# Kernel optimization log

Hardware: AMD Instinct MI355X
Metric: run time of the kernel (lower is better)

## Reference

```python
import jax, jax.numpy as jnp
import numpy as np

N_TRACK = 50000
N_LANE = 50000
N_ATT = N_TRACK + N_LANE
NP_T = 1000000
NP_L = 500000
E_ATT = 1600000
D_TRACK = 4
D_LANE = 2
D_ATT = 10
HEADS = 30
D_OUT = 2
EPS = 1e-5
NEG_SLOPE = 0.2


def _mlp(x, W, b, g, beta):
    # Linear -> LayerNorm -> ReLU (matches MLP module)
    h = x @ W + b
    mu = h.mean(-1, keepdims=True)
    var = ((h - mu) ** 2).mean(-1, keepdims=True)
    h = (h - mu) * jax.lax.rsqrt(var + EPS) * g + beta
    return jax.nn.relu(h)


def _seg_max0(x, ids, n):
    # DGL max-reduce; nodes with no in-edges get 0
    m = jax.ops.segment_max(x, ids, num_segments=n, indices_are_sorted=True)
    return jnp.where(jnp.isfinite(m), m, 0.0)


def setup_inputs() -> dict:
    key = jax.random.key(0)
    ks = jax.random.split(key, 16)
    g = lambda i, shape, s=1.0: jax.random.normal(ks[i], shape, jnp.float32) * s
    return {
        'track_point_feats': g(0, (NP_T, D_TRACK)),
        'lane_point_feats': g(1, (NP_L, D_LANE)),
        'point_track_id': jnp.sort(jax.random.randint(ks[2], (NP_T,), 0, N_TRACK)),
        'point_lane_id': jnp.sort(jax.random.randint(ks[3], (NP_L,), 0, N_LANE)),
        'att_src': jax.random.randint(ks[4], (E_ATT,), 0, N_ATT),
        'att_dst': jnp.sort(jax.random.randint(ks[5], (E_ATT,), 0, N_ATT)),
        'track_mlp_W': g(6, (D_TRACK, D_TRACK), 0.5),
        'track_mlp_b': jnp.zeros((D_TRACK,), jnp.float32),
        'track_ln_g': jnp.ones((D_TRACK,), jnp.float32),
        'track_ln_b': jnp.zeros((D_TRACK,), jnp.float32),
        'track_out_W': g(7, (D_TRACK, D_ATT), 0.5),
        'track_out_b': jnp.zeros((D_ATT,), jnp.float32),
        'lane_mlp_W': g(8, (D_LANE, D_LANE), 0.5),
        'lane_mlp_b': jnp.zeros((D_LANE,), jnp.float32),
        'lane_ln_g': jnp.ones((D_LANE,), jnp.float32),
        'lane_ln_b': jnp.zeros((D_LANE,), jnp.float32),
        'lane_out_W': g(9, (D_LANE, D_ATT), 0.5),
        'lane_out_b': jnp.zeros((D_ATT,), jnp.float32),
        'gat_fc_W': g(10, (D_ATT, HEADS * D_OUT), 0.3),
        'gat_attn_l': g(11, (HEADS, D_OUT), 0.3),
        'gat_attn_r': g(12, (HEADS, D_OUT), 0.3),
        'gat_bias': jnp.zeros((HEADS * D_OUT,), jnp.float32),
    }


def reference(track_point_feats, lane_point_feats, point_track_id, point_lane_id,
              att_src, att_dst,
              track_mlp_W, track_mlp_b, track_ln_g, track_ln_b, track_out_W, track_out_b,
              lane_mlp_W, lane_mlp_b, lane_ln_g, lane_ln_b, lane_out_W, lane_out_b,
              gat_fc_W, gat_attn_l, gat_attn_r, gat_bias):
    # SubTrackModel: per-point MLP -> segment max over point->track -> linear
    track_pool = _seg_max0(_mlp(track_point_feats, track_mlp_W, track_mlp_b, track_ln_g, track_ln_b),
                           point_track_id, N_TRACK)
    track_feats = track_pool @ track_out_W + track_out_b  # [N_TRACK, 10]
    # SubLaneModel
    lane_pool = _seg_max0(_mlp(lane_point_feats, lane_mlp_W, lane_mlp_b, lane_ln_g, lane_ln_b),
                          point_lane_id, N_LANE)
    lane_feats = lane_pool @ lane_out_W + lane_out_b  # [N_LANE, 10]
    feats = jnp.concatenate([track_feats, lane_feats], axis=0)  # [N_ATT, 10]

    # GATConv (30 heads, out 2)
    h = (feats @ gat_fc_W).reshape(N_ATT, HEADS, D_OUT)
    el = jnp.einsum('nhd,hd->nh', h, gat_attn_l)
    er = jnp.einsum('nhd,hd->nh', h, gat_attn_r)
    e = jax.nn.leaky_relu(el[att_src] + er[att_dst], NEG_SLOPE)  # [E, H]
    m = jax.ops.segment_max(e, att_dst, num_segments=N_ATT, indices_are_sorted=True)
    m = jnp.where(jnp.isfinite(m), m, 0.0)
    ee = jnp.exp(e - m[att_dst])
    den = jax.ops.segment_sum(ee, att_dst, num_segments=N_ATT, indices_are_sorted=True)
    alpha = ee / den[att_dst]  # edge softmax over incoming edges per dst
    msg = alpha[:, :, None] * h[att_src]  # [E, H, D_OUT]
    out = jax.ops.segment_sum(msg, att_dst, num_segments=N_ATT, indices_are_sorted=True)
    out = out.reshape(N_ATT, HEADS * D_OUT) + gat_bias
    return out[:N_TRACK]
```

## Files before the change

kernel.cpp:

```cpp
#include <hip/hip_runtime.h>
#include <hip/hip_bf16.h>
#include <math.h>

#define N_TRACK 50000
#define N_LANE  50000
#define N_ATT   (N_TRACK + N_LANE)
#define NP_T    1000000
#define NP_L    500000
#define E_ATT   1600000
#define HEADS   30
#define EPS     1e-5f
#define NEG_SLOPE 0.2f

#define REC_STRIDE 96

__global__ void point_kernel(const float4* __restrict__ xt, const float2* __restrict__ xl,
                             const int* __restrict__ idt, const int* __restrict__ idl,
                             const float* __restrict__ tW, const float* __restrict__ tb,
                             const float* __restrict__ tg, const float* __restrict__ tbeta,
                             const float* __restrict__ lW, const float* __restrict__ lb,
                             const float* __restrict__ lg, const float* __restrict__ lbeta,
                             float* __restrict__ pool_t, float* __restrict__ pool_l) {
    int tid = blockIdx.x * blockDim.x + threadIdx.x;
    int lane = threadIdx.x & 63;
    int id = -1;
    float y0 = 0.f, y1 = 0.f, y2 = 0.f, y3 = 0.f;
    if (tid < NP_T) {
        float4 xv = xt[tid];
        float h[4];
        #pragma unroll
        for (int j = 0; j < 4; j++)
            h[j] = xv.x * tW[0*4+j] + xv.y * tW[1*4+j] + xv.z * tW[2*4+j] + xv.w * tW[3*4+j] + tb[j];
        float mu = 0.25f * (h[0] + h[1] + h[2] + h[3]);
        float var = 0.f;
        #pragma unroll
        for (int j = 0; j < 4; j++) { float d = h[j] - mu; var += d * d; }
        var *= 0.25f;
        float r = rsqrtf(var + EPS);
        y0 = fmaxf((h[0] - mu) * r * tg[0] + tbeta[0], 0.f);
        y1 = fmaxf((h[1] - mu) * r * tg[1] + tbeta[1], 0.f);
        y2 = fmaxf((h[2] - mu) * r * tg[2] + tbeta[2], 0.f);
        y3 = fmaxf((h[3] - mu) * r * tg[3] + tbeta[3], 0.f);
        id = idt[tid];
    } else if (tid < NP_T + NP_L) {
        int t = tid - NP_T;
        float2 xv = xl[t];
        float h0 = xv.x * lW[0] + xv.y * lW[2] + lb[0];
        float h1 = xv.x * lW[1] + xv.y * lW[3] + lb[1];
        float mu = 0.5f * (h0 + h1);
        float var = 0.5f * ((h0 - mu) * (h0 - mu) + (h1 - mu) * (h1 - mu));
        float r = rsqrtf(var + EPS);
        y0 = fmaxf((h0 - mu) * r * lg[0] + lbeta[0], 0.f);
        y1 = fmaxf((h1 - mu) * r * lg[1] + lbeta[1], 0.f);
        id = N_TRACK + idl[t];
    }
    #pragma unroll
    for (int d = 1; d < 64; d <<= 1) {
        int oid = __shfl_down(id, d, 64);
        float o0 = __shfl_down(y0, d, 64);
        float o1 = __shfl_down(y1, d, 64);
        float o2 = __shfl_down(y2, d, 64);
        float o3 = __shfl_down(y3, d, 64);
        if (oid == id) {
            y0 = fmaxf(y0, o0); y1 = fmaxf(y1, o1);
            y2 = fmaxf(y2, o2); y3 = fmaxf(y3, o3);
        }
    }
    int pid = __shfl_up(id, 1, 64);
    bool head = (lane == 0) || (pid != id);
    if (id >= 0 && head) {
        if (id < N_TRACK) {
            unsigned int* p = (unsigned int*)&pool_t[(size_t)id * 4];
            atomicMax(p + 0, __float_as_uint(y0));
            atomicMax(p + 1, __float_as_uint(y1));
            atomicMax(p + 2, __float_as_uint(y2));
            atomicMax(p + 3, __float_as_uint(y3));
        } else {
            unsigned int* p = (unsigned int*)&pool_l[(size_t)(id - N_TRACK) * 2];
            atomicMax(p + 0, __float_as_uint(y0));
            atomicMax(p + 1, __float_as_uint(y1));
        }
    }
}

__global__ void node_kernel(const float* __restrict__ pool_t, const float* __restrict__ pool_l,
                            const float* __restrict__ tW, const float* __restrict__ tb,
                            const float* __restrict__ lW, const float* __restrict__ lb,
                            const float* __restrict__ fcW, const float* __restrict__ attn_l,
                            const int* __restrict__ att_dst,
                            float* __restrict__ packed, int* __restrict__ off) {
    int i = blockIdx.x * blockDim.x + threadIdx.x;

    if (i <= N_TRACK) {
        int lo = 0, hi = E_ATT;
        while (lo < hi) {
            int mid = (lo + hi) >> 1;
            if (att_dst[mid] < i) lo = mid + 1; else hi = mid;
        }
        off[i] = lo;
    }
    if (i >= N_ATT) return;

    float f[10];
    if (i < N_TRACK) {
        const float4 p = *(const float4*)(pool_t + (size_t)i * 4);
        #pragma unroll
        for (int j = 0; j < 10; j++)
            f[j] = p.x * tW[0*10+j] + p.y * tW[1*10+j] + p.z * tW[2*10+j] + p.w * tW[3*10+j] + tb[j];
    } else {
        const float2 p = *(const float2*)(pool_l + (size_t)(i - N_TRACK) * 2);
        #pragma unroll
        for (int j = 0; j < 10; j++)
            f[j] = p.x * lW[0*10+j] + p.y * lW[1*10+j] + lb[j];
    }

    float rec[REC_STRIDE];
    #pragma unroll
    for (int c = 0; c < 60; c++) {
        float acc = 0.f;
        #pragma unroll
        for (int k = 0; k < 10; k++) acc += f[k] * fcW[k * 60 + c];
        rec[3 * (c >> 1) + 1 + (c & 1)] = acc;
    }
    #pragma unroll
    for (int hh = 0; hh < HEADS; hh++)
        rec[3 * hh] = rec[3 * hh + 1] * attn_l[2 * hh] + rec[3 * hh + 2] * attn_l[2 * hh + 1];
    #pragma unroll
    for (int q = 90; q < 96; q++) rec[q] = 0.f;

    float4* rp = (float4*)(packed + (size_t)i * REC_STRIDE);
    #pragma unroll
    for (int q = 0; q < 24; q++)
        rp[q] = make_float4(rec[4*q], rec[4*q+1], rec[4*q+2], rec[4*q+3]);
}

__global__ void edge_kernel(const int* __restrict__ src, const int* __restrict__ off,
                            const float* __restrict__ packed,
                            const float* __restrict__ attn_r, const float* __restrict__ bias,
                            float* __restrict__ out) {
    int grp = blockIdx.x * 8 + (threadIdx.x >> 5);
    int hh = threadIdx.x & 31;
    if (grp >= N_TRACK || hh >= HEADS) return;

    const float* prec = packed + (size_t)grp * REC_STRIDE + hh * 3;
    float er = prec[1] * attn_r[2 * hh] + prec[2] * attn_r[2 * hh + 1];

    int s = off[grp], e = off[grp + 1];
    float m = -INFINITY, den = 0.f, n0 = 0.f, n1 = 0.f;

    for (int kk = s; kk < e; kk += 8) {
        int lim = e - kk;
        int sv[8];
        #pragma unroll
        for (int j = 0; j < 8; j++) sv[j] = src[kk + (j < lim ? j : 0)];
        float e_[8], a_[8], b_[8];
        #pragma unroll
        for (int j = 0; j < 8; j++) {
            const float* p = packed + (size_t)sv[j] * REC_STRIDE + hh * 3;
            e_[j] = p[0]; a_[j] = p[1]; b_[j] = p[2];
        }
        #pragma unroll
        for (int j = 0; j < 8; j++) {
            if (j < lim) {
                float ev = e_[j] + er;
                ev = (ev > 0.f) ? ev : NEG_SLOPE * ev;
                float nm = fmaxf(m, ev);
                float sc = __expf(m - nm);
                float w  = __expf(ev - nm);
                den = den * sc + w;
                n0  = n0 * sc + w * a_[j];
                n1  = n1 * sc + w * b_[j];
                m = nm;
            }
        }
    }

    float o0 = 0.f, o1 = 0.f;
    if (den > 0.f) {
        float inv = 1.f / den;
        o0 = n0 * inv; o1 = n1 * inv;
    }
    ((float2*)out)[(size_t)grp * HEADS + hh] =
        make_float2(o0 + bias[2 * hh], o1 + bias[2 * hh + 1]);
}

extern "C" void kernel_launch(void* const* d_in, const int* in_sizes, int n_in,
                              void* d_out, int out_size, void* d_ws, size_t ws_size,
                              hipStream_t stream) {
    const float4* track_pts = (const float4*)d_in[0];
    const float2* lane_pts  = (const float2*)d_in[1];
    const int* pt_track_id  = (const int*)d_in[2];
    const int* pt_lane_id   = (const int*)d_in[3];
    const int* att_src      = (const int*)d_in[4];
    const int* att_dst      = (const int*)d_in[5];
    const float* track_mlp_W = (const float*)d_in[6];
    const float* track_mlp_b = (const float*)d_in[7];
    const float* track_ln_g  = (const float*)d_in[8];
    const float* track_ln_b  = (const float*)d_in[9];
    const float* track_out_W = (const float*)d_in[10];
    const float* track_out_b = (const float*)d_in[11];
    const float* lane_mlp_W  = (const float*)d_in[12];
    const float* lane_mlp_b  = (const float*)d_in[13];
    const float* lane_ln_g   = (const float*)d_in[14];
    const float* lane_ln_b   = (const float*)d_in[15];
    const float* lane_out_W  = (const float*)d_in[16];
    const float* lane_out_b  = (const float*)d_in[17];
    const float* gat_fc_W    = (const float*)d_in[18];
    const float* gat_attn_l  = (const float*)d_in[19];
    const float* gat_attn_r  = (const float*)d_in[20];
    const float* gat_bias    = (const float*)d_in[21];
    float* out = (float*)d_out;

    float* pool_t = (float*)d_ws;
    float* pool_l = pool_t + 200000;
    int*   off    = (int*)(pool_l + 100000);
    float* packed = (float*)(off + 50004);

    hipMemsetAsync(d_ws, 0, 300000 * sizeof(float), stream);

    point_kernel<<<(NP_T + NP_L + 255) / 256, 256, 0, stream>>>(
        track_pts, lane_pts, pt_track_id, pt_lane_id,
        track_mlp_W, track_mlp_b, track_ln_g, track_ln_b,
        lane_mlp_W, lane_mlp_b, lane_ln_g, lane_ln_b,
        pool_t, pool_l);
    node_kernel<<<(N_ATT + 255) / 256, 256, 0, stream>>>(
        pool_t, pool_l, track_out_W, track_out_b, lane_out_W, lane_out_b,
        gat_fc_W, gat_attn_l, att_dst, packed, off);
    edge_kernel<<<(N_TRACK + 7) / 8, 256, 0, stream>>>(
        att_src, off, packed, gat_attn_r, gat_bias, out);
}
```

Measured before the change: 209.2 us.

## Store per-node head features as packed bf16 and recompute el in edge loop

After: 174.0 us. 16.8% less time.

```diff
diff --git a/kernel.cpp b/kernel.cpp
--- a/kernel.cpp
+++ b/kernel.cpp
@@ -12,7 +12,7 @@
 #define EPS     1e-5f
 #define NEG_SLOPE 0.2f
 
-#define REC_STRIDE 96
+#define REC_DW 32
 
 __global__ void point_kernel(const float4* __restrict__ xt, const float2* __restrict__ xl,
                              const int* __restrict__ idt, const int* __restrict__ idl,
@@ -86,9 +86,9 @@
 __global__ void node_kernel(const float* __restrict__ pool_t, const float* __restrict__ pool_l,
                             const float* __restrict__ tW, const float* __restrict__ tb,
                             const float* __restrict__ lW, const float* __restrict__ lb,
-                            const float* __restrict__ fcW, const float* __restrict__ attn_l,
+                            const float* __restrict__ fcW,
                             const int* __restrict__ att_dst,
-                            float* __restrict__ packed, int* __restrict__ off) {
+                            unsigned int* __restrict__ hpack, int* __restrict__ off) {
     int i = blockIdx.x * blockDim.x + threadIdx.x;
 
     if (i <= N_TRACK) {
@@ -114,62 +114,67 @@
             f[j] = p.x * lW[0*10+j] + p.y * lW[1*10+j] + lb[j];
     }
 
-    float rec[REC_STRIDE];
+    unsigned int rec[REC_DW];
     #pragma unroll
-    for (int c = 0; c < 60; c++) {
-        float acc = 0.f;
-        #pragma unroll
-        for (int k = 0; k < 10; k++) acc += f[k] * fcW[k * 60 + c];
-        rec[3 * (c >> 1) + 1 + (c & 1)] = acc;
-    }
+    for (int hh = 0; hh < HEADS; hh++) {
+        float a0 = 0.f, a1 = 0.f;
+        #pragma unroll
+        for (int k = 0; k < 10; k++) {
+            a0 += f[k] * fcW[k * 60 + 2 * hh];
+            a1 += f[k] * fcW[k * 60 + 2 * hh + 1];
+        }
+        unsigned int b0 = (unsigned int)__hip_bfloat16_raw(__float2bfloat16(a0)).x;
+        unsigned int b1 = (unsigned int)__hip_bfloat16_raw(__float2bfloat16(a1)).x;
+        rec[hh] = b0 | (b1 << 16);
+    }
+    rec[30] = 0u; rec[31] = 0u;
+
+    uint4* rp = (uint4*)(hpack + (size_t)i * REC_DW);
     #pragma unroll
-    for (int hh = 0; hh < HEADS; hh++)
-        rec[3 * hh] = rec[3 * hh + 1] * attn_l[2 * hh] + rec[3 * hh + 2] * attn_l[2 * hh + 1];
-    #pragma unroll
-    for (int q = 90; q < 96; q++) rec[q] = 0.f;
-
-    float4* rp = (float4*)(packed + (size_t)i * REC_STRIDE);
-    #pragma unroll
-    for (int q = 0; q < 24; q++)
-        rp[q] = make_float4(rec[4*q], rec[4*q+1], rec[4*q+2], rec[4*q+3]);
+    for (int q = 0; q < 8; q++)
+        rp[q] = make_uint4(rec[4*q], rec[4*q+1], rec[4*q+2], rec[4*q+3]);
 }
 
 __global__ void edge_kernel(const int* __restrict__ src, const int* __restrict__ off,
-                            const float* __restrict__ packed,
-                            const float* __restrict__ attn_r, const float* __restrict__ bias,
-                            float* __restrict__ out) {
+                            const unsigned int* __restrict__ hpack,
+                            const float* __restrict__ attn_l, const float* __restrict__ attn_r,
+                            const float* __restrict__ bias, float* __restrict__ out) {
     int grp = blockIdx.x * 8 + (threadIdx.x >> 5);
     int hh = threadIdx.x & 31;
     if (grp >= N_TRACK || hh >= HEADS) return;
 
-    const float* prec = packed + (size_t)grp * REC_STRIDE + hh * 3;
-    float er = prec[1] * attn_r[2 * hh] + prec[2] * attn_r[2 * hh + 1];
+    float al0 = attn_l[2 * hh], al1 = attn_l[2 * hh + 1];
+    float ar0 = attn_r[2 * hh], ar1 = attn_r[2 * hh + 1];
+
+    unsigned int dd = hpack[(size_t)grp * REC_DW + hh];
+    float hd0 = __uint_as_float(dd << 16);
+    float hd1 = __uint_as_float(dd & 0xffff0000u);
+    float er = hd0 * ar0 + hd1 * ar1;
 
     int s = off[grp], e = off[grp + 1];
     float m = -INFINITY, den = 0.f, n0 = 0.f, n1 = 0.f;
 
-    for (int kk = s; kk < e; kk += 8) {
+    for (int kk = s; kk < e; kk += 16) {
         int lim = e - kk;
-        int sv[8];
-        #pragma unroll
-        for (int j = 0; j < 8; j++) sv[j] = src[kk + (j < lim ? j : 0)];
-        float e_[8], a_[8], b_[8];
-        #pragma unroll
-        for (int j = 0; j < 8; j++) {
-            const float* p = packed + (size_t)sv[j] * REC_STRIDE + hh * 3;
-            e_[j] = p[0]; a_[j] = p[1]; b_[j] = p[2];
-        }
-        #pragma unroll
-        for (int j = 0; j < 8; j++) {
+        int sv[16];
+        #pragma unroll
+        for (int j = 0; j < 16; j++) sv[j] = src[kk + (j < lim ? j : 0)];
+        unsigned int d[16];
+        #pragma unroll
+        for (int j = 0; j < 16; j++) d[j] = hpack[(size_t)sv[j] * REC_DW + hh];
+        #pragma unroll
+        for (int j = 0; j < 16; j++) {
             if (j < lim) {
-                float ev = e_[j] + er;
+                float h0 = __uint_as_float(d[j] << 16);
+                float h1 = __uint_as_float(d[j] & 0xffff0000u);
+                float ev = h0 * al0 + h1 * al1 + er;
                 ev = (ev > 0.f) ? ev : NEG_SLOPE * ev;
                 float nm = fmaxf(m, ev);
                 float sc = __expf(m - nm);
                 float w  = __expf(ev - nm);
                 den = den * sc + w;
-                n0  = n0 * sc + w * a_[j];
-                n1  = n1 * sc + w * b_[j];
+                n0  = n0 * sc + w * h0;
+                n1  = n1 * sc + w * h1;
                 m = nm;
             }
         }
@@ -214,7 +219,7 @@
     float* pool_t = (float*)d_ws;
     float* pool_l = pool_t + 200000;
     int*   off    = (int*)(pool_l + 100000);
-    float* packed = (float*)(off + 50004);
+    unsigned int* hpack = (unsigned int*)(off + 50016);
 
     hipMemsetAsync(d_ws, 0, 300000 * sizeof(float), stream);
 
@@ -225,7 +230,7 @@
         pool_t, pool_l);
     node_kernel<<<(N_ATT + 255) / 256, 256, 0, stream>>>(
         pool_t, pool_l, track_out_W, track_out_b, lane_out_W, lane_out_b,
-        gat_fc_W, gat_attn_l, att_dst, packed, off);
+        gat_fc_W, att_dst, hpack, off);
     edge_kernel<<<(N_TRACK + 7) / 8, 256, 0, stream>>>(
-        att_src, off, packed, gat_attn_r, gat_bias, out);
-}
+        att_src, off, hpack, gat_attn_l, gat_attn_r, gat_bias, out);
+}
```
